# Optimization experiments

Hardware: AMD Instinct MI355X
Metric: run time of the kernel (lower is better)

Reference implementation:

```python
import jax, jax.numpy as jnp
import numpy as np

B, N, H, W, C_OUT = 4, 480000, 1024, 1024, 64
PR = (0.0, -39.68, -3.0, 69.12, 39.68, 1.0)  # point cloud range [x0,y0,z0,x1,y1,z1]
BN_EPS = 1e-5


def setup_inputs():
    key = jax.random.key(0)
    ks = iter(jax.random.split(key, 48))
    bidx = jax.random.randint(next(ks), (N,), 0, B).astype(jnp.float32)
    px = jax.random.uniform(next(ks), (N,), minval=PR[0], maxval=PR[3])
    py = jax.random.uniform(next(ks), (N,), minval=PR[1], maxval=PR[4])
    pz = jax.random.uniform(next(ks), (N,), minval=PR[2], maxval=PR[5])
    pi = jax.random.uniform(next(ks), (N,))
    points = jnp.stack([bidx, px, py, pz, pi], axis=1)  # [N,5]

    def w(shape):
        return jax.random.normal(next(ks), shape, jnp.float32) * 0.1

    def bnp(c):
        return (1.0 + 0.1 * jax.random.normal(next(ks), (c,), jnp.float32),
                0.1 * jax.random.normal(next(ks), (c,), jnp.float32),
                0.1 * jax.random.normal(next(ks), (c,), jnp.float32),
                jax.random.uniform(next(ks), (c,), minval=0.5, maxval=1.5))

    g0, be0, m0, v0 = bnp(8)
    g1, be1, m1, v1 = bnp(16)
    g2, be2, m2, v2 = bnp(32)
    g3, be3, m3, v3 = bnp(C_OUT)
    return {
        'points': points, 'batch_size': B,
        'w0': w((8, 2, 3, 3)), 'b0': w((8,)),
        'g0': g0, 'be0': be0, 'm0': m0, 'v0': v0,
        'w1': w((16, 1, 3, 3)), 'b1': w((16,)),  # groups=8 conv: 16 out, 8 in groups
        'g1': g1, 'be1': be1, 'm1': m1, 'v1': v1,
        'wdw': w((16, 1, 3, 3)), 'bdw': w((16,)),
        'wpw': w((32, 16, 1, 1)), 'bpw': w((32,)),
        'g2': g2, 'be2': be2, 'm2': m2, 'v2': v2,
        'w3': w((C_OUT, 32, 3, 3)), 'b3': w((C_OUT,)),
        'g3': g3, 'be3': be3, 'm3': m3, 'v3': v3,
    }


def conv2d(x, wt, b, groups=1, pad=1):
    out = jax.lax.conv_general_dilated(
        x, wt, (1, 1), [(pad, pad), (pad, pad)],
        feature_group_count=groups,
        dimension_numbers=('NCHW', 'OIHW', 'NCHW'))
    return out + b[None, :, None, None]


def bn(x, g, be, m, v):
    s = g * jax.lax.rsqrt(v + BN_EPS)
    return x * s[None, :, None, None] + (be - m * s)[None, :, None, None]


def maxpool2(x):
    return jax.lax.reduce_window(x, -jnp.inf, jax.lax.max,
                                 (1, 1, 2, 2), (1, 1, 2, 2), 'VALID')


def channel_shuffle(x, groups):
    b, c, h, w = x.shape
    return x.reshape(b, groups, c // groups, h, w).transpose(0, 2, 1, 3, 4).reshape(b, c, h, w)


def rasterize(points, batch_size):
    # points: [N,5] = (batch_idx, x, y, z, intensity)
    x_scale = W / (PR[3] - PR[0])
    y_scale = H / (PR[4] - PR[1])
    # PR[0]==0 -> no x shift (matches the source's branch)
    xp = (points[:, 1] * x_scale).astype(jnp.int32)  # trunc toward zero like torch .to(int)
    yp = ((points[:, 2] + (PR[4] - PR[1]) / 2) * y_scale).astype(jnp.int32)
    valid = (xp >= 0) & (xp < W) & (yp >= 0) & (yp < H)
    bi = jnp.where(valid, points[:, 0].astype(jnp.int32), batch_size)  # invalid -> OOB, dropped
    xi = jnp.where(valid, xp, W)
    yi = jnp.where(valid, yp, H)
    bev_z = jnp.full((batch_size, H, W), -10.0, jnp.float32)
    bev_z = bev_z.at[bi, yi, xi].max(points[:, 3], mode='drop')
    bev_i = jnp.zeros((batch_size, H, W), jnp.float32)
    bev_i = bev_i.at[bi, yi, xi].max(points[:, 4], mode='drop')
    return jnp.stack([bev_z, bev_i], axis=1)  # [B,2,H,W]


def reference(points, batch_size, w0, b0, g0, be0, m0, v0, w1, b1, g1, be1, m1, v1,
              wdw, bdw, wpw, bpw, g2, be2, m2, v2, w3, b3, g3, be3, m3, v3):
    x = rasterize(points, batch_size)
    x = jax.nn.relu(bn(conv2d(x, w0, b0), g0, be0, m0, v0))          # x_conv1
    x = maxpool2(x)
    x = jax.nn.relu(bn(conv2d(x, w1, b1, groups=8), g1, be1, m1, v1))  # x_conv2
    x = maxpool2(x)
    x = conv2d(x, wdw, bdw, groups=16)      # depthwise
    x = channel_shuffle(x, 16)              # identity when groups==channels, kept for faithfulness
    x = conv2d(x, wpw, bpw, pad=0)          # pointwise 16->32
    x = jax.nn.relu(bn(x, g2, be2, m2, v2))
    x = jax.nn.relu(bn(conv2d(x, w3, b3), g3, be3, m3, v3))          # x_conv3
    x = maxpool2(x)                         # x_conv4 == spatial_features
    return x
```

## Files before the change

### kernel.cpp

```cpp
#include <hip/hip_runtime.h>
#include <cstddef>

#define H_IN 1024
#define W_IN 1024
#define BN_EPS 1e-5f

typedef float f32x4 __attribute__((ext_vector_type(4)));
typedef _Float16 f16x8 __attribute__((ext_vector_type(8)));

__device__ __forceinline__ void atomicMaxF(float* addr, float val) {
    if (val >= 0.0f) {
        atomicMax((int*)addr, __float_as_int(val));
    } else {
        atomicMin((unsigned int*)addr, __float_as_uint(val));
    }
}

__global__ void k_init_bev(float* __restrict__ bev) {
    size_t i = (size_t)blockIdx.x * blockDim.x + threadIdx.x;
    int plane = (int)((i >> 20) & 1);
    bev[i] = plane == 0 ? -10.0f : 0.0f;
}

__global__ void k_rasterize(const float* __restrict__ pts, float* __restrict__ bev, int n) {
    int i = blockIdx.x * blockDim.x + threadIdx.x;
    if (i >= n) return;
    float fb  = pts[(size_t)i*5+0];
    float px  = pts[(size_t)i*5+1];
    float py  = pts[(size_t)i*5+2];
    float pz  = pts[(size_t)i*5+3];
    float pit = pts[(size_t)i*5+4];
    const float XS = (float)(1024.0/69.12);
    const float YS = (float)(1024.0/79.36);
    int xp = (int)(px * XS);
    int yp = (int)((py + 39.68f) * YS);
    if (xp < 0 || xp >= W_IN || yp < 0 || yp >= H_IN) return;
    int b = (int)fb;
    size_t off = (size_t)(b*2) * (H_IN*(size_t)W_IN) + (size_t)yp*W_IN + xp;
    atomicMaxF(bev + off, pz);
    atomicMaxF(bev + off + (size_t)H_IN*W_IN, pit);
}

__global__ __launch_bounds__(256, 4) void k_conv1(
                        const float* __restrict__ bev, const float* __restrict__ w0,
                        const float* __restrict__ b0, const float* __restrict__ g0,
                        const float* __restrict__ be0, const float* __restrict__ m0,
                        const float* __restrict__ v0, float* __restrict__ out) {
    __shared__ float wS[144];
    __shared__ float sS[8], tS[8];
    int t = threadIdx.x;
    if (t < 144) wS[t] = w0[t];
    if (t < 8) {
        float s = g0[t] / sqrtf(v0[t] + BN_EPS);
        sS[t] = s;
        tS[t] = (b0[t] - m0[t]) * s + be0[t];
    }
    __syncthreads();
    int idx = blockIdx.x * 256 + t;
    int x = idx & 511, y = (idx >> 9) & 511, b = idx >> 18;
    const float* base = bev + (size_t)b * 2 * H_IN * W_IN;
    float in[2][4][4];
    #pragma unroll
    for (int c = 0; c < 2; c++)
        #pragma unroll
        for (int r = 0; r < 4; r++) {
            int iy = 2*y - 1 + r;
            #pragma unroll
            for (int cc = 0; cc < 4; cc++) {
                int ix = 2*x - 1 + cc;
                in[c][r][cc] = (iy >= 0 && iy < H_IN && ix >= 0 && ix < W_IN)
                    ? base[(size_t)c*H_IN*W_IN + (size_t)iy*W_IN + ix] : 0.0f;
            }
        }
    float* ob = out + (size_t)b * 8 * 512 * 512 + (size_t)y*512 + x;
    #pragma unroll
    for (int oc = 0; oc < 8; oc++) {
        float mx = 0.0f;
        #pragma unroll
        for (int py = 0; py < 2; py++)
            #pragma unroll
            for (int px = 0; px < 2; px++) {
                float acc = 0.0f;
                #pragma unroll
                for (int c = 0; c < 2; c++)
                    #pragma unroll
                    for (int kh = 0; kh < 3; kh++)
                        #pragma unroll
                        for (int kw = 0; kw < 3; kw++)
                            acc += in[c][py+kh][px+kw] * wS[((oc*2+c)*3+kh)*3+kw];
                acc = fmaxf(acc * sS[oc] + tS[oc], 0.0f);
                mx = fmaxf(mx, acc);
            }
        ob[(size_t)oc*512*512] = mx;
    }
}

__global__ __launch_bounds__(256, 4) void k_conv2(
                        const float* __restrict__ x1, const float* __restrict__ w1,
                        const float* __restrict__ b1, const float* __restrict__ g1,
                        const float* __restrict__ be1, const float* __restrict__ m1,
                        const float* __restrict__ v1, float* __restrict__ out) {
    __shared__ float wS[144];
    __shared__ float sS[16], tS[16];
    int t = threadIdx.x;
    if (t < 144) wS[t] = w1[t];
    if (t < 16) {
        float s = g1[t] / sqrtf(v1[t] + BN_EPS);
        sS[t] = s;
        tS[t] = (b1[t] - m1[t]) * s + be1[t];
    }
    __syncthreads();
    int idx = blockIdx.x * 256 + t;
    int x = idx & 255, y = (idx >> 8) & 255, b = idx >> 16;
    const float* base = x1 + (size_t)b * 8 * 512 * 512;
    float* ob = out + (size_t)b * 16 * 256 * 256 + (size_t)y*256 + x;
    #pragma unroll
    for (int g = 0; g < 8; g++) {
        float p[4][4];
        #pragma unroll
        for (int r = 0; r < 4; r++) {
            int iy = 2*y - 1 + r;
            #pragma unroll
            for (int c = 0; c < 4; c++) {
                int ix = 2*x - 1 + c;
                p[r][c] = (iy >= 0 && iy < 512 && ix >= 0 && ix < 512)
                    ? base[(size_t)g*512*512 + (size_t)iy*512 + ix] : 0.0f;
            }
        }
        #pragma unroll
        for (int sub = 0; sub < 2; sub++) {
            int oc = g*2 + sub;
            float mx = 0.0f;
            #pragma unroll
            for (int py = 0; py < 2; py++)
                #pragma unroll
                for (int px = 0; px < 2; px++) {
                    float acc = 0.0f;
                    #pragma unroll
                    for (int kh = 0; kh < 3; kh++)
                        #pragma unroll
                        for (int kw = 0; kw < 3; kw++)
                            acc += p[py+kh][px+kw] * wS[(oc*3+kh)*3+kw];
                    acc = fmaxf(acc * sS[oc] + tS[oc], 0.0f);
                    mx = fmaxf(mx, acc);
                }
            ob[(size_t)oc*256*256] = mx;
        }
    }
}

__global__ __launch_bounds__(256, 4) void k_dwpw(
                       const float* __restrict__ x2, const float* __restrict__ wdw,
                       const float* __restrict__ bdw, const float* __restrict__ wpw,
                       const float* __restrict__ bpw, const float* __restrict__ g2,
                       const float* __restrict__ be2, const float* __restrict__ m2,
                       const float* __restrict__ v2, _Float16* __restrict__ out) {
    __shared__ float patch[16*10*36];
    __shared__ float wdwS[144];
    __shared__ float bdwS[16];
    __shared__ float wpwS[512];
    __shared__ float sS[32], tS[32];
    int t = threadIdx.x;
    if (t < 144) wdwS[t] = wdw[t];
    if (t < 16) bdwS[t] = bdw[t];
    for (int i = t; i < 512; i += 256) wpwS[i] = wpw[i];
    if (t < 32) {
        float s = g2[t] / sqrtf(v2[t] + BN_EPS);
        sS[t] = s;
        tS[t] = (bpw[t] - m2[t]) * s + be2[t];
    }

    int bi = blockIdx.x;
    int tx = bi & 7, ty = (bi >> 3) & 31, b = bi >> 8;
    int x0 = tx * 32, y0 = ty * 8;
    const float* base = x2 + (size_t)b * 16 * 256 * 256;

    for (int i = t; i < 16*10*34; i += 256) {
        int ic = i / 340;
        int rem = i - ic * 340;
        int r = rem / 34, c = rem - r * 34;
        int gy = y0 - 1 + r, gx = x0 - 1 + c;
        patch[(ic*10 + r)*36 + c] =
            (gy >= 0 && gy < 256 && gx >= 0 && gx < 256)
                ? base[(size_t)ic*65536 + (size_t)gy*256 + gx] : 0.0f;
    }
    __syncthreads();

    int px = t & 31, pyy = t >> 5;
    int x = x0 + px, y = y0 + pyy;

    float dv[16];
    #pragma unroll
    for (int ic = 0; ic < 16; ic++) {
        float d = bdwS[ic];
        #pragma unroll
        for (int r = 0; r < 3; r++)
            #pragma unroll
            for (int c = 0; c < 3; c++)
                d += patch[(ic*10 + pyy + r)*36 + px + c] * wdwS[ic*9 + r*3 + c];
        dv[ic] = d;
    }

    _Float16* ob = out + ((size_t)((b*256 + y)*256 + x)) * 32;
    #pragma unroll
    for (int q = 0; q < 4; q++) {
        f16x8 ov;
        #pragma unroll
        for (int j = 0; j < 8; j++) {
            int oc = q*8 + j;
            float a = 0.0f;
            #pragma unroll
            for (int ic = 0; ic < 16; ic++)
                a += dv[ic] * wpwS[oc*16+ic];
            ov[j] = (_Float16)fmaxf(a*sS[oc] + tS[oc], 0.0f);
        }
        *(f16x8*)(ob + q*8) = ov;
    }
}

__global__ void k_wprep(const float* __restrict__ w3, const float* __restrict__ b3,
                        const float* __restrict__ g3, const float* __restrict__ be3,
                        const float* __restrict__ m3, const float* __restrict__ v3,
                        _Float16* __restrict__ wh, float* __restrict__ tv) {
    int t = threadIdx.x;
    for (int i = t; i < 9*64*32; i += 256) {
        int khw = i >> 11;
        int rem = i & 2047;
        int oc = rem >> 5, ic = rem & 31;
        int kh = khw / 3, kw = khw % 3;
        float s = g3[oc] / sqrtf(v3[oc] + BN_EPS);
        wh[i] = (_Float16)(w3[((oc*32 + ic)*3 + kh)*3 + kw] * s);
    }
    if (t < 64) {
        float s = g3[t] / sqrtf(v3[t] + BN_EPS);
        tv[t] = (b3[t] - m3[t]) * s + be3[t];
    }
}

__global__ __launch_bounds__(256, 2) void k_conv3m(const _Float16* __restrict__ xh,
                                                   const _Float16* __restrict__ wh,
                                                   const float* __restrict__ tv,
                                                   float* __restrict__ out) {
    __shared__ _Float16 As[4*66*40];
    int t = threadIdx.x;
    int lane = t & 63, w = t >> 6;
    int l15 = lane & 15, l4 = lane >> 4;
    int bi = blockIdx.x;
    int xt = bi & 3, yg = (bi >> 2) & 31, b = bi >> 7;
    int x0 = xt * 64;

    f16x8 Bf[9][4];
    #pragma unroll
    for (int khw = 0; khw < 9; khw++)
        #pragma unroll
        for (int g = 0; g < 4; g++)
            Bf[khw][g] = *(const f16x8*)(wh + ((khw*64 + g*16 + l15)*32 + 8*l4));

    float tvv[4];
    #pragma unroll
    for (int g = 0; g < 4; g++) tvv[g] = tv[g*16 + l15];

    for (int ti = 0; ti < 4; ti++) {
        int ypool = yg*4 + ti;
        int y0 = ypool*2;
        __syncthreads();
        for (int s = t; s < 264; s += 256) {
            int row = s / 66, px = s % 66;
            int gy = y0 - 1 + row, gx = x0 - 1 + px;
            float4* dst = (float4*)&As[(row*66 + px)*40];
            if (gy >= 0 && gy < 256 && gx >= 0 && gx < 256) {
                const float4* src = (const float4*)(xh + ((size_t)((b*256 + gy)*256 + gx)) * 32);
                #pragma unroll
                for (int j = 0; j < 4; j++) dst[j] = src[j];
            } else {
                float4 z = make_float4(0.f, 0.f, 0.f, 0.f);
                #pragma unroll
                for (int j = 0; j < 4; j++) dst[j] = z;
            }
        }
        __syncthreads();

        f32x4 acc[2][4];
        #pragma unroll
        for (int f = 0; f < 2; f++)
            #pragma unroll
            for (int g = 0; g < 4; g++)
                acc[f][g] = (f32x4){0.f, 0.f, 0.f, 0.f};

        #pragma unroll
        for (int kh = 0; kh < 3; kh++)
            #pragma unroll
            for (int kw = 0; kw < 3; kw++) {
                f16x8 Af[2];
                #pragma unroll
                for (int f = 0; f < 2; f++) {
                    int row = f + kh;
                    int px = w*16 + l15 + kw;
                    Af[f] = *(const f16x8*)&As[(row*66 + px)*40 + 8*l4];
                }
                #pragma unroll
                for (int f = 0; f < 2; f++)
                    #pragma unroll
                    for (int g = 0; g < 4; g++)
                        acc[f][g] = __builtin_amdgcn_mfma_f32_16x16x32_f16(
                            Af[f], Bf[kh*3+kw][g], acc[f][g], 0, 0, 0);
            }

        #pragma unroll
        for (int g = 0; g < 4; g++) {
            int oc = g*16 + l15;
            #pragma unroll
            for (int q = 0; q < 2; q++) {
                float v0 = fmaxf(fmaxf(acc[0][g][2*q]   + tvv[g], 0.f),
                                 fmaxf(acc[0][g][2*q+1] + tvv[g], 0.f));
                float v1 = fmaxf(fmaxf(acc[1][g][2*q]   + tvv[g], 0.f),
                                 fmaxf(acc[1][g][2*q+1] + tvv[g], 0.f));
                int px = x0/2 + w*8 + 2*l4 + q;
                out[(((size_t)b*64 + oc)*128 + ypool)*128 + px] = fmaxf(v0, v1);
            }
        }
    }
}

extern "C" void kernel_launch(void* const* d_in, const int* in_sizes, int n_in,
                              void* d_out, int out_size, void* d_ws, size_t ws_size,
                              hipStream_t stream) {
    const float* points = (const float*)d_in[0];
    int n = in_sizes[0] / 5;
    const float* w0  = (const float*)d_in[2];
    const float* b0  = (const float*)d_in[3];
    const float* g0  = (const float*)d_in[4];
    const float* be0 = (const float*)d_in[5];
    const float* m0  = (const float*)d_in[6];
    const float* v0  = (const float*)d_in[7];
    const float* w1  = (const float*)d_in[8];
    const float* b1  = (const float*)d_in[9];
    const float* g1  = (const float*)d_in[10];
    const float* be1 = (const float*)d_in[11];
    const float* m1  = (const float*)d_in[12];
    const float* v1  = (const float*)d_in[13];
    const float* wdw = (const float*)d_in[14];
    const float* bdw = (const float*)d_in[15];
    const float* wpw = (const float*)d_in[16];
    const float* bpw = (const float*)d_in[17];
    const float* g2  = (const float*)d_in[18];
    const float* be2 = (const float*)d_in[19];
    const float* m2  = (const float*)d_in[20];
    const float* v2  = (const float*)d_in[21];
    const float* w3  = (const float*)d_in[22];
    const float* b3  = (const float*)d_in[23];
    const float* g3  = (const float*)d_in[24];
    const float* be3 = (const float*)d_in[25];
    const float* m3  = (const float*)d_in[26];
    const float* v3  = (const float*)d_in[27];

    float* ws  = (float*)d_ws;
    float* bev = ws;
    float* x1  = ws + 8388608;
    float* x2  = bev;
    _Float16* x3h = (_Float16*)(ws + 8388608);
    _Float16* wh  = (_Float16*)ws;
    float* tv  = ws + 9216;
    float* outp = (float*)d_out;

    k_init_bev<<<32768, 256, 0, stream>>>(bev);
    k_rasterize<<<(n + 255)/256, 256, 0, stream>>>(points, bev, n);
    k_conv1<<<4096, 256, 0, stream>>>(bev, w0, b0, g0, be0, m0, v0, x1);
    k_conv2<<<1024, 256, 0, stream>>>(x1, w1, b1, g1, be1, m1, v1, x2);
    k_dwpw<<<1024, 256, 0, stream>>>(x2, wdw, bdw, wpw, bpw, g2, be2, m2, v2, x3h);
    k_wprep<<<1, 256, 0, stream>>>(w3, b3, g3, be3, m3, v3, wh, tv);
    k_conv3m<<<512, 256, 0, stream>>>(x3h, wh, tv, outp);
}
```

Baseline: 151.4 us.

## Store conv1 output in fp16, parallelize weight prep, stage conv3 halo once

The conv1 output is stored as fp16 and conv2 reads fp16, halving the bytes of the largest intermediate written and read. k_wprep now runs on 9 blocks with coalesced reads and moves ahead in the stream, with its buffers relocated so they do not overlap the other intermediates. k_conv3m loads one 10-row halo tile into LDS once instead of four 4-row tiles with barriers, which cuts redundant global loads and syncs but raises LDS use per block. The fp16 intermediate adds rounding error to the activations.

```diff
diff --git a/kernel.cpp b/kernel.cpp
--- a/kernel.cpp
+++ b/kernel.cpp
@@ -45,7 +45,7 @@
                         const float* __restrict__ bev, const float* __restrict__ w0,
                         const float* __restrict__ b0, const float* __restrict__ g0,
                         const float* __restrict__ be0, const float* __restrict__ m0,
-                        const float* __restrict__ v0, float* __restrict__ out) {
+                        const float* __restrict__ v0, _Float16* __restrict__ out) {
     __shared__ float wS[144];
     __shared__ float sS[8], tS[8];
     int t = threadIdx.x;
@@ -72,7 +72,7 @@
                     ? base[(size_t)c*H_IN*W_IN + (size_t)iy*W_IN + ix] : 0.0f;
             }
         }
-    float* ob = out + (size_t)b * 8 * 512 * 512 + (size_t)y*512 + x;
+    _Float16* ob = out + (size_t)b * 8 * 512 * 512 + (size_t)y*512 + x;
     #pragma unroll
     for (int oc = 0; oc < 8; oc++) {
         float mx = 0.0f;
@@ -91,12 +91,12 @@
                 acc = fmaxf(acc * sS[oc] + tS[oc], 0.0f);
                 mx = fmaxf(mx, acc);
             }
-        ob[(size_t)oc*512*512] = mx;
+        ob[(size_t)oc*512*512] = (_Float16)mx;
     }
 }
 
 __global__ __launch_bounds__(256, 4) void k_conv2(
-                        const float* __restrict__ x1, const float* __restrict__ w1,
+                        const _Float16* __restrict__ x1, const float* __restrict__ w1,
                         const float* __restrict__ b1, const float* __restrict__ g1,
                         const float* __restrict__ be1, const float* __restrict__ m1,
                         const float* __restrict__ v1, float* __restrict__ out) {
@@ -112,7 +112,7 @@
     __syncthreads();
     int idx = blockIdx.x * 256 + t;
     int x = idx & 255, y = (idx >> 8) & 255, b = idx >> 16;
-    const float* base = x1 + (size_t)b * 8 * 512 * 512;
+    const _Float16* base = x1 + (size_t)b * 8 * 512 * 512;
     float* ob = out + (size_t)b * 16 * 256 * 256 + (size_t)y*256 + x;
     #pragma unroll
     for (int g = 0; g < 8; g++) {
@@ -124,7 +124,7 @@
             for (int c = 0; c < 4; c++) {
                 int ix = 2*x - 1 + c;
                 p[r][c] = (iy >= 0 && iy < 512 && ix >= 0 && ix < 512)
-                    ? base[(size_t)g*512*512 + (size_t)iy*512 + ix] : 0.0f;
+                    ? (float)base[(size_t)g*512*512 + (size_t)iy*512 + ix] : 0.0f;
             }
         }
         #pragma unroll
@@ -144,7 +144,7 @@
                     acc = fmaxf(acc * sS[oc] + tS[oc], 0.0f);
                     mx = fmaxf(mx, acc);
                 }
-            ob[(size_t)oc*256*256] = mx;
+            ob[(size_t)oc*65536] = mx;
         }
     }
 }
@@ -222,18 +222,18 @@
                         const float* __restrict__ g3, const float* __restrict__ be3,
                         const float* __restrict__ m3, const float* __restrict__ v3,
                         _Float16* __restrict__ wh, float* __restrict__ tv) {
-    int t = threadIdx.x;
-    for (int i = t; i < 9*64*32; i += 256) {
-        int khw = i >> 11;
-        int rem = i & 2047;
-        int oc = rem >> 5, ic = rem & 31;
-        int kh = khw / 3, kw = khw % 3;
-        float s = g3[oc] / sqrtf(v3[oc] + BN_EPS);
-        wh[i] = (_Float16)(w3[((oc*32 + ic)*3 + kh)*3 + kw] * s);
-    }
+    __shared__ float sSh[64];
+    int t = threadIdx.x;
     if (t < 64) {
         float s = g3[t] / sqrtf(v3[t] + BN_EPS);
-        tv[t] = (b3[t] - m3[t]) * s + be3[t];
+        sSh[t] = s;
+        if (blockIdx.x == 0) tv[t] = (b3[t] - m3[t]) * s + be3[t];
+    }
+    __syncthreads();
+    int khw = blockIdx.x;
+    for (int i = t; i < 2048; i += 256) {
+        int oc = i >> 5;
+        wh[khw*2048 + i] = (_Float16)(w3[(size_t)i*9 + khw] * sSh[oc]);
     }
 }
 
@@ -241,13 +241,14 @@
                                                    const _Float16* __restrict__ wh,
                                                    const float* __restrict__ tv,
                                                    float* __restrict__ out) {
-    __shared__ _Float16 As[4*66*40];
+    __shared__ _Float16 As[10*66*40];
     int t = threadIdx.x;
     int lane = t & 63, w = t >> 6;
     int l15 = lane & 15, l4 = lane >> 4;
     int bi = blockIdx.x;
     int xt = bi & 3, yg = (bi >> 2) & 31, b = bi >> 7;
     int x0 = xt * 64;
+    int y0 = yg * 8;
 
     f16x8 Bf[9][4];
     #pragma unroll
@@ -260,26 +261,24 @@
     #pragma unroll
     for (int g = 0; g < 4; g++) tvv[g] = tv[g*16 + l15];
 
+    for (int s = t; s < 660; s += 256) {
+        int row = s / 66, px = s - row*66;
+        int gy = y0 - 1 + row, gx = x0 - 1 + px;
+        float4* dst = (float4*)&As[(row*66 + px)*40];
+        if (gy >= 0 && gy < 256 && gx >= 0 && gx < 256) {
+            const float4* src = (const float4*)(xh + ((size_t)((b*256 + gy)*256 + gx)) * 32);
+            #pragma unroll
+            for (int j = 0; j < 4; j++) dst[j] = src[j];
+        } else {
+            float4 z = make_float4(0.f, 0.f, 0.f, 0.f);
+            #pragma unroll
+            for (int j = 0; j < 4; j++) dst[j] = z;
+        }
+    }
+    __syncthreads();
+
     for (int ti = 0; ti < 4; ti++) {
         int ypool = yg*4 + ti;
-        int y0 = ypool*2;
-        __syncthreads();
-        for (int s = t; s < 264; s += 256) {
-            int row = s / 66, px = s % 66;
-            int gy = y0 - 1 + row, gx = x0 - 1 + px;
-            float4* dst = (float4*)&As[(row*66 + px)*40];
-            if (gy >= 0 && gy < 256 && gx >= 0 && gx < 256) {
-                const float4* src = (const float4*)(xh + ((size_t)((b*256 + gy)*256 + gx)) * 32);
-                #pragma unroll
-                for (int j = 0; j < 4; j++) dst[j] = src[j];
-            } else {
-                float4 z = make_float4(0.f, 0.f, 0.f, 0.f);
-                #pragma unroll
-                for (int j = 0; j < 4; j++) dst[j] = z;
-            }
-        }
-        __syncthreads();
-
         f32x4 acc[2][4];
         #pragma unroll
         for (int f = 0; f < 2; f++)
@@ -294,7 +293,7 @@
                 f16x8 Af[2];
                 #pragma unroll
                 for (int f = 0; f < 2; f++) {
-                    int row = f + kh;
+                    int row = 2*ti + f + kh;
                     int px = w*16 + l15 + kw;
                     Af[f] = *(const f16x8*)&As[(row*66 + px)*40 + 8*l4];
                 }
@@ -356,18 +355,18 @@
 
     float* ws  = (float*)d_ws;
     float* bev = ws;
-    float* x1  = ws + 8388608;
-    float* x2  = bev;
+    _Float16* x1h = (_Float16*)(ws + 8388608);
+    float* x2  = ws;
     _Float16* x3h = (_Float16*)(ws + 8388608);
-    _Float16* wh  = (_Float16*)ws;
-    float* tv  = ws + 9216;
+    _Float16* wh  = (_Float16*)(ws + 16777216);
+    float* tv  = ws + 16786432;
     float* outp = (float*)d_out;
 
+    k_wprep<<<9, 256, 0, stream>>>(w3, b3, g3, be3, m3, v3, wh, tv);
     k_init_bev<<<32768, 256, 0, stream>>>(bev);
     k_rasterize<<<(n + 255)/256, 256, 0, stream>>>(points, bev, n);
-    k_conv1<<<4096, 256, 0, stream>>>(bev, w0, b0, g0, be0, m0, v0, x1);
-    k_conv2<<<1024, 256, 0, stream>>>(x1, w1, b1, g1, be1, m1, v1, x2);
+    k_conv1<<<4096, 256, 0, stream>>>(bev, w0, b0, g0, be0, m0, v0, x1h);
+    k_conv2<<<1024, 256, 0, stream>>>(x1h, w1, b1, g1, be1, m1, v1, x2);
     k_dwpw<<<1024, 256, 0, stream>>>(x2, wdw, bdw, wpw, bpw, g2, be2, m2, v2, x3h);
-    k_wprep<<<1, 256, 0, stream>>>(w3, b3, g3, be3, m3, v3, wh, tv);
     k_conv3m<<<512, 256, 0, stream>>>(x3h, wh, tv, outp);
 }
```

Measured after the change: 147.0 us. 1.03x faster.
